# Kernel optimization log

Hardware: AMD Instinct MI355X
Metric: run time of the kernel (lower is better)

The kernel has to match this reference:

```python
import jax, jax.numpy as jnp
import numpy as np

B, S, K = 8, 128, 12          # batch, seq len, nPredicts
DAR, DENC = 256, 256          # AR dim, encoder dim
NNEG = 128                    # negativeSamplingExt
W = S - K                     # windowSize


def setup_inputs() -> dict:
    key = jax.random.key(0)
    k1, k2, k3, k4, k5 = jax.random.split(key, 5)
    cFeature = jax.random.normal(k1, (B, S, DAR), dtype=jnp.float32)
    encodedData = jax.random.normal(k2, (B, S, DENC), dtype=jnp.float32)
    # stacked bias-free Linear weights, one per prediction step k
    Wpred = jax.random.normal(k3, (K, DENC, DAR), dtype=jnp.float32) / jnp.sqrt(DAR)
    n_idx = NNEG * W * B
    batchIdx = jax.random.randint(k4, (n_idx,), 0, B, dtype=jnp.int32)
    seqIdx = jax.random.randint(k5, (n_idx,), 1, S, dtype=jnp.int32)  # low=1 as in torch
    return {"cFeature": cFeature, "encodedData": encodedData, "Wpred": Wpred,
            "batchIdx": batchIdx, "seqIdx": seqIdx}


def reference(cFeature, encodedData, Wpred, batchIdx, seqIdx):
    c = cFeature[:, :W]                                   # (B, W, DAR)
    flat = encodedData.reshape(-1, DENC)                  # (B*S, DENC)

    # sampleClean: baseIdx arange(W) broadcast over (B, NNEG, W) then flattened
    base = jnp.tile(jnp.arange(W, dtype=jnp.int32), B * NNEG)
    seq = (seqIdx + base) % S
    ext = seq + batchIdx * S
    negExt = flat[ext].reshape(B, NNEG, W, DENC)          # irregular gather, ~121 MB

    # per-k linear prediction: locC[k] = c @ Wpred[k].T
    locC = jnp.einsum('bwd,ked->kbwe', c, Wpred)          # (K, B, W, DENC)

    # positives: encodedData[:, k:k+W] for k = 1..K
    pos = jnp.stack([encodedData[:, k:k + W] for k in range(1, K + 1)])  # (K, B, W, DENC)

    # (locC * candidates).mean(dim=feature) == dot / DENC
    posScore = jnp.einsum('kbwe,kbwe->kbw', locC, pos) / DENC           # (K, B, W)
    negScore = jnp.einsum('kbwe,bnwe->kbnw', locC, negExt) / DENC       # (K, B, N, W)

    logits = jnp.concatenate([posScore[:, :, None, :], negScore], axis=2)  # (K, B, 1+N, W)
    logits = jnp.transpose(logits, (0, 1, 3, 2)).reshape(K, B * W, 1 + NNEG)

    # cross entropy with label 0 (positive at class index 0)
    lse = jax.nn.logsumexp(logits, axis=-1)               # (K, B*W)
    losses = jnp.mean(lse - logits[..., 0], axis=-1)      # (K,)
    accs = jnp.mean((jnp.argmax(logits, axis=-1) == 0).astype(jnp.float32), axis=-1)
    return losses[None, :], accs[None, :]                  # (1, K), (1, K)
```

## Files before the change

### kernel.cpp

```cpp
#include <hip/hip_runtime.h>
#include <math.h>

#define B_    8
#define S_    128
#define K_    12
#define DAR_  256
#define DENC_ 256
#define NNEG_ 128
#define W_    116
#define BW_   928

typedef __attribute__((ext_vector_type(8))) short short8;
typedef __attribute__((ext_vector_type(4))) float floatx4;

static __device__ __forceinline__ unsigned short f2bf(float f) {
    union { float f; unsigned int u; } v; v.f = f;
    return (unsigned short)((v.u + 0x7FFFu + ((v.u >> 16) & 1u)) >> 16);
}

__global__ __launch_bounds__(256) void cast_all(
    const float* __restrict__ enc, const float* __restrict__ cf,
    const float* __restrict__ wp,
    unsigned short* __restrict__ ench, unsigned short* __restrict__ cfh,
    unsigned short* __restrict__ wph)
{
    const int g = blockIdx.x * 256 + threadIdx.x;
    const float* src; unsigned short* dst; int off;
    if (g < 32768)      { src = enc; dst = ench; off = g * 8; }
    else if (g < 65536) { src = cf;  dst = cfh;  off = (g - 32768) * 8; }
    else                { src = wp;  dst = wph;  off = (g - 65536) * 8; }
    float4 v0 = *(const float4*)(src + off);
    float4 v1 = *(const float4*)(src + off + 4);
    uint4 o;
    o.x = f2bf(v0.x) | ((unsigned)f2bf(v0.y) << 16);
    o.y = f2bf(v0.z) | ((unsigned)f2bf(v0.w) << 16);
    o.z = f2bf(v1.x) | ((unsigned)f2bf(v1.y) << 16);
    o.w = f2bf(v1.z) | ((unsigned)f2bf(v1.w) << 16);
    *(uint4*)(dst + off) = o;
}

__global__ __launch_bounds__(256) void stage1_mfma(
    const unsigned short* __restrict__ cfh,
    const unsigned short* __restrict__ wph,
    unsigned short* __restrict__ locCh)
{
    __shared__ unsigned short Bh[64 * 256];

    const int tid = threadIdx.x;
    const int mt = blockIdx.x;
    const int nt = blockIdx.y;
    const int k  = blockIdx.z;

    const int lane = tid & 63, wv = tid >> 6;
    const int l15 = lane & 15, quad = lane >> 4;

    const int am = mt * 64 + wv * 16 + l15;
    const bool avalid = (am < BW_);
    short8 a[8];
    if (avalid) {
        const int b = am / W_, w = am - b * W_;
        const unsigned short* arow = cfh + (size_t)(b * S_ + w) * 256;
#pragma unroll
        for (int kt = 0; kt < 8; ++kt)
            a[kt] = *(const short8*)(arow + kt * 32 + quad * 8);
    } else {
#pragma unroll
        for (int kt = 0; kt < 8; ++kt) a[kt] = short8{0,0,0,0,0,0,0,0};
    }

#pragma unroll
    for (int i = 0; i < 8; ++i) {
        const int flat = i * 256 + tid;
        const int row = flat >> 5, ch = flat & 31;
        const int e = nt * 64 + row;
        uint4 bv = *(const uint4*)(wph + ((size_t)(k * 256 + e) * 256 + ch * 8));
        *(uint4*)&Bh[(row * 32 + (ch ^ (row & 7))) * 8] = bv;
    }
    __syncthreads();

    floatx4 acc[4];
#pragma unroll
    for (int n4 = 0; n4 < 4; ++n4) {
        floatx4 c = {0.f, 0.f, 0.f, 0.f};
        const int bn = n4 * 16 + l15;
#pragma unroll
        for (int kt = 0; kt < 8; ++kt) {
            const int ch = kt * 4 + quad;
            short8 bfrag = *(const short8*)&Bh[(bn * 32 + (ch ^ (bn & 7))) * 8];
            c = __builtin_amdgcn_mfma_f32_16x16x32_bf16(a[kt], bfrag, c, 0, 0, 0);
        }
        acc[n4] = c;
    }

#pragma unroll
    for (int n4 = 0; n4 < 4; ++n4) {
        const int e = nt * 64 + n4 * 16 + l15;
#pragma unroll
        for (int r = 0; r < 4; ++r) {
            const int bwo = mt * 64 + wv * 16 + quad * 4 + r;
            if (bwo < BW_)
                locCh[((size_t)k * BW_ + bwo) * 256 + e] = f2bf(acc[r < 0 ? 0 : n4][r]);
        }
    }
}

__global__ __launch_bounds__(256) void stage2_mfma(
    const unsigned short* __restrict__ ench,
    const unsigned short* __restrict__ locCh,
    const int* __restrict__ batchIdx,
    const int* __restrict__ seqIdx,
    float* __restrict__ part)
{
    __shared__ int   idxL[144];
    __shared__ float sc[K_ * 132];

    const int tid = threadIdx.x;
    const int bw = blockIdx.x;
    const int b = bw / W_, w = bw - b * W_;

    const int lane = tid & 63, wv = tid >> 6;
    const int l15 = lane & 15, quad = lane >> 4;

    const int m = (l15 < K_) ? l15 : (K_ - 1);
    const unsigned short* arow = locCh + ((size_t)m * BW_ + bw) * 256;
    short8 a[8];
#pragma unroll
    for (int kt = 0; kt < 8; ++kt)
        a[kt] = *(const short8*)(arow + kt * 32 + quad * 8);

    if (tid < NNEG_) {
        const int ii = (b * NNEG_ + tid) * W_ + w;
        const int bi = batchIdx[ii];
        int si = seqIdx[ii] + w;
        if (si >= S_) si -= S_;
        idxL[tid] = bi * S_ + si;
    } else if (tid < 140) {
        idxL[tid] = b * S_ + w + 1 + (tid - 128);
    }
    __syncthreads();

    floatx4 accT[3];
#pragma unroll
    for (int u = 0; u < 3; ++u) {
        const int t = wv + u * 4;
        floatx4 c = {0.f, 0.f, 0.f, 0.f};
        if (t < 9) {
            const int n = t * 16 + l15;
            const int nn = (n < 140) ? n : 128;
            const unsigned short* brow = ench + (size_t)idxL[nn] * 256;
#pragma unroll
            for (int kt = 0; kt < 8; ++kt) {
                short8 bfrag = *(const short8*)(brow + kt * 32 + quad * 8);
                c = __builtin_amdgcn_mfma_f32_16x16x32_bf16(a[kt], bfrag, c, 0, 0, 0);
            }
        }
        accT[u] = c;
    }

    const float inv = 1.0f / 256.0f;
#pragma unroll
    for (int u = 0; u < 3; ++u) {
        const int t = wv + u * 4;
        if (t < 9) {
#pragma unroll
            for (int r = 0; r < 4; ++r) {
                const int mm = quad * 4 + r;
                if (mm < K_) {
                    const float val = accT[u][r] * inv;
                    if (t < 8)           sc[mm * 132 + t * 16 + l15] = val;
                    else if (l15 == mm)  sc[mm * 132 + 128] = val;
                }
            }
        }
    }
    __syncthreads();

    for (int k = wv; k < K_; k += 4) {
        const float x0  = sc[k * 132 + lane];
        const float x1  = sc[k * 132 + 64 + lane];
        const float pos = sc[k * 132 + 128];
        float mn = fmaxf(x0, x1);
#pragma unroll
        for (int o = 1; o < 64; o <<= 1) mn = fmaxf(mn, __shfl_xor(mn, o, 64));
        const float m2 = fmaxf(mn, pos);
        float s = __expf(x0 - m2) + __expf(x1 - m2);
#pragma unroll
        for (int o = 1; o < 64; o <<= 1) s += __shfl_xor(s, o, 64);
        if (lane == 0) {
            const float lse = m2 + __logf(s + __expf(pos - m2));
            part[k * BW_ + bw]        = lse - pos;
            part[(K_ + k) * BW_ + bw] = (pos >= mn) ? 1.0f : 0.0f;
        }
    }
}

__global__ __launch_bounds__(256) void stage3_reduce(
    const float* __restrict__ part, float* __restrict__ out)
{
    __shared__ float wsum[4];
    const int o = blockIdx.x, tid = threadIdx.x;
    float s = 0.f;
    for (int i = tid; i < BW_; i += 256) s += part[o * BW_ + i];
#pragma unroll
    for (int off = 1; off < 64; off <<= 1) s += __shfl_xor(s, off, 64);
    if ((tid & 63) == 0) wsum[tid >> 6] = s;
    __syncthreads();
    if (tid == 0)
        out[o] = (wsum[0] + wsum[1] + wsum[2] + wsum[3]) / (float)BW_;
}

extern "C" void kernel_launch(void* const* d_in, const int* in_sizes, int n_in,
                              void* d_out, int out_size, void* d_ws, size_t ws_size,
                              hipStream_t stream) {
    const float* cFeat    = (const float*)d_in[0];
    const float* enc      = (const float*)d_in[1];
    const float* Wp       = (const float*)d_in[2];
    const int*   batchIdx = (const int*)d_in[3];
    const int*   seqIdx   = (const int*)d_in[4];
    float* out = (float*)d_out;

    unsigned short* ench  = (unsigned short*)d_ws;
    unsigned short* cfh   = ench + 262144;
    unsigned short* wph   = cfh + 262144;
    unsigned short* locCh = wph + 786432;
    float*          part  = (float*)(locCh + (size_t)K_ * BW_ * 256);

    hipLaunchKernelGGL(cast_all, dim3(640), dim3(256), 0, stream,
                       enc, cFeat, Wp, ench, cfh, wph);
    hipLaunchKernelGGL(stage1_mfma, dim3(15, 4, 12), dim3(256), 0, stream,
                       cfh, wph, locCh);
    hipLaunchKernelGGL(stage2_mfma, dim3(BW_), dim3(256), 0, stream,
                       ench, locCh, batchIdx, seqIdx, part);
    hipLaunchKernelGGL(stage3_reduce, dim3(24), dim3(256), 0, stream,
                       part, out);
}
```

Baseline: 92.93 us.

## Precompute transposed negative indices, enlarge stage1 tile, prefetch stage2 gathers, nontemporal stores

Negative-sample indices are now computed once in the prep kernel into a contiguous per-(b,w) table, replacing strided loads of batchIdx/seqIdx in stage2. Stage1 now computes 128 rows per block, reusing each LDS B fragment across two A tiles. Stage2 issues all gathered encoder row loads before the MFMAs, so memory latency overlaps. Nontemporal loads and stores and a launch_bounds occupancy hint are added throughout. These changes raise register pressure, and the extra prep pass adds some traffic of its own.

Result: slower. 98.99 us (+6.5%).

```diff
diff --git a/kernel.cpp b/kernel.cpp
--- a/kernel.cpp
+++ b/kernel.cpp
@@ -9,37 +9,56 @@
 #define NNEG_ 128
 #define W_    116
 #define BW_   928
+#define NIDX_ 118784
 
 typedef __attribute__((ext_vector_type(8))) short short8;
 typedef __attribute__((ext_vector_type(4))) float floatx4;
+typedef __attribute__((ext_vector_type(4))) unsigned int uintx4;
 
 static __device__ __forceinline__ unsigned short f2bf(float f) {
     union { float f; unsigned int u; } v; v.f = f;
     return (unsigned short)((v.u + 0x7FFFu + ((v.u >> 16) & 1u)) >> 16);
 }
 
-__global__ __launch_bounds__(256) void cast_all(
-    const float* __restrict__ enc, const float* __restrict__ cf,
-    const float* __restrict__ wp,
-    unsigned short* __restrict__ ench, unsigned short* __restrict__ cfh,
-    unsigned short* __restrict__ wph)
-{
-    const int g = blockIdx.x * 256 + threadIdx.x;
-    const float* src; unsigned short* dst; int off;
-    if (g < 32768)      { src = enc; dst = ench; off = g * 8; }
-    else if (g < 65536) { src = cf;  dst = cfh;  off = (g - 32768) * 8; }
-    else                { src = wp;  dst = wph;  off = (g - 65536) * 8; }
-    float4 v0 = *(const float4*)(src + off);
-    float4 v1 = *(const float4*)(src + off + 4);
-    uint4 o;
+static __device__ __forceinline__ uintx4 pack2(float4 v0, float4 v1) {
+    uintx4 o;
     o.x = f2bf(v0.x) | ((unsigned)f2bf(v0.y) << 16);
     o.y = f2bf(v0.z) | ((unsigned)f2bf(v0.w) << 16);
     o.z = f2bf(v1.x) | ((unsigned)f2bf(v1.y) << 16);
     o.w = f2bf(v1.z) | ((unsigned)f2bf(v1.w) << 16);
-    *(uint4*)(dst + off) = o;
-}
-
-__global__ __launch_bounds__(256) void stage1_mfma(
+    return o;
+}
+
+__global__ __launch_bounds__(256) void k0_prep(
+    const float* __restrict__ enc, const float* __restrict__ cf,
+    const float* __restrict__ wp,
+    const int* __restrict__ batchIdx, const int* __restrict__ seqIdx,
+    unsigned short* __restrict__ ench, unsigned short* __restrict__ cfh,
+    unsigned short* __restrict__ wph, int* __restrict__ idxT)
+{
+    const int tid0 = blockIdx.x * 256 + threadIdx.x;
+    for (int g = tid0; g < 163840; g += 192 * 256) {
+        const float* src; unsigned short* dst; int off;
+        if (g < 32768)      { src = enc; dst = ench; off = g * 8; }
+        else if (g < 65536) { src = cf;  dst = cfh;  off = (g - 32768) * 8; }
+        else                { src = wp;  dst = wph;  off = (g - 65536) * 8; }
+        float4 v0 = *(const float4*)(src + off);
+        float4 v1 = *(const float4*)(src + off + 4);
+        uintx4 o = pack2(v0, v1);
+        __builtin_nontemporal_store(o, (uintx4*)(dst + off));
+    }
+    for (int j = tid0; j < NIDX_; j += 192 * 256) {
+        const int n = j & 127, bw = j >> 7;
+        const int b = bw / W_, w = bw - b * W_;
+        const int ii = (b * NNEG_ + n) * W_ + w;
+        const int bi = batchIdx[ii];
+        int si = seqIdx[ii] + w;
+        if (si >= S_) si -= S_;
+        __builtin_nontemporal_store(bi * S_ + si, idxT + j);
+    }
+}
+
+__global__ __launch_bounds__(256, 2) void stage1_mfma(
     const unsigned short* __restrict__ cfh,
     const unsigned short* __restrict__ wph,
     unsigned short* __restrict__ locCh)
@@ -54,61 +73,69 @@
     const int lane = tid & 63, wv = tid >> 6;
     const int l15 = lane & 15, quad = lane >> 4;
 
-    const int am = mt * 64 + wv * 16 + l15;
-    const bool avalid = (am < BW_);
-    short8 a[8];
-    if (avalid) {
-        const int b = am / W_, w = am - b * W_;
+    short8 a[2][8];
+#pragma unroll
+    for (int im = 0; im < 2; ++im) {
+        const int row = mt * 128 + wv * 32 + im * 16 + l15;
+        const int rowc = (row < BW_) ? row : (BW_ - 1);
+        const int b = rowc / W_, w = rowc - b * W_;
         const unsigned short* arow = cfh + (size_t)(b * S_ + w) * 256;
 #pragma unroll
         for (int kt = 0; kt < 8; ++kt)
-            a[kt] = *(const short8*)(arow + kt * 32 + quad * 8);
-    } else {
-#pragma unroll
-        for (int kt = 0; kt < 8; ++kt) a[kt] = short8{0,0,0,0,0,0,0,0};
+            a[im][kt] = *(const short8*)(arow + kt * 32 + quad * 8);
     }
 
 #pragma unroll
     for (int i = 0; i < 8; ++i) {
         const int flat = i * 256 + tid;
         const int row = flat >> 5, ch = flat & 31;
-        const int e = nt * 64 + row;
-        uint4 bv = *(const uint4*)(wph + ((size_t)(k * 256 + e) * 256 + ch * 8));
-        *(uint4*)&Bh[(row * 32 + (ch ^ (row & 7))) * 8] = bv;
-    }
-    __syncthreads();
-
-    floatx4 acc[4];
+        uintx4 bv = *(const uintx4*)(wph + ((size_t)(k * 256 + nt * 64 + row) * 256 + ch * 8));
+        *(uintx4*)&Bh[(row * 32 + (ch ^ (row & 7))) * 8] = bv;
+    }
+    __syncthreads();
+
+    floatx4 acc[2][4];
 #pragma unroll
     for (int n4 = 0; n4 < 4; ++n4) {
-        floatx4 c = {0.f, 0.f, 0.f, 0.f};
         const int bn = n4 * 16 + l15;
+        short8 bfrag[8];
 #pragma unroll
         for (int kt = 0; kt < 8; ++kt) {
             const int ch = kt * 4 + quad;
-            short8 bfrag = *(const short8*)&Bh[(bn * 32 + (ch ^ (bn & 7))) * 8];
-            c = __builtin_amdgcn_mfma_f32_16x16x32_bf16(a[kt], bfrag, c, 0, 0, 0);
-        }
-        acc[n4] = c;
-    }
-
-#pragma unroll
-    for (int n4 = 0; n4 < 4; ++n4) {
-        const int e = nt * 64 + n4 * 16 + l15;
-#pragma unroll
-        for (int r = 0; r < 4; ++r) {
-            const int bwo = mt * 64 + wv * 16 + quad * 4 + r;
-            if (bwo < BW_)
-                locCh[((size_t)k * BW_ + bwo) * 256 + e] = f2bf(acc[r < 0 ? 0 : n4][r]);
-        }
-    }
-}
-
-__global__ __launch_bounds__(256) void stage2_mfma(
+            bfrag[kt] = *(const short8*)&Bh[(bn * 32 + (ch ^ (bn & 7))) * 8];
+        }
+#pragma unroll
+        for (int im = 0; im < 2; ++im) {
+            floatx4 c = (n4 == 0) ? floatx4{0.f, 0.f, 0.f, 0.f} : acc[im][n4];
+            c = acc[im][n4];
+            c = floatx4{0.f, 0.f, 0.f, 0.f};
+#pragma unroll
+            for (int kt = 0; kt < 8; ++kt)
+                c = __builtin_amdgcn_mfma_f32_16x16x32_bf16(a[im][kt], bfrag[kt], c, 0, 0, 0);
+            acc[im][n4] = c;
+        }
+    }
+
+#pragma unroll
+    for (int im = 0; im < 2; ++im) {
+#pragma unroll
+        for (int n4 = 0; n4 < 4; ++n4) {
+            const int e = nt * 64 + n4 * 16 + l15;
+#pragma unroll
+            for (int r = 0; r < 4; ++r) {
+                const int bwo = mt * 128 + wv * 32 + im * 16 + quad * 4 + r;
+                if (bwo < BW_)
+                    __builtin_nontemporal_store(f2bf(acc[im][n4][r]),
+                        locCh + ((size_t)k * BW_ + bwo) * 256 + e);
+            }
+        }
+    }
+}
+
+__global__ __launch_bounds__(256, 2) void stage2_mfma(
     const unsigned short* __restrict__ ench,
     const unsigned short* __restrict__ locCh,
-    const int* __restrict__ batchIdx,
-    const int* __restrict__ seqIdx,
+    const int* __restrict__ idxT,
     float* __restrict__ part)
 {
     __shared__ int   idxL[144];
@@ -126,34 +153,32 @@
     short8 a[8];
 #pragma unroll
     for (int kt = 0; kt < 8; ++kt)
-        a[kt] = *(const short8*)(arow + kt * 32 + quad * 8);
-
-    if (tid < NNEG_) {
-        const int ii = (b * NNEG_ + tid) * W_ + w;
-        const int bi = batchIdx[ii];
-        int si = seqIdx[ii] + w;
-        if (si >= S_) si -= S_;
-        idxL[tid] = bi * S_ + si;
-    } else if (tid < 140) {
-        idxL[tid] = b * S_ + w + 1 + (tid - 128);
-    }
-    __syncthreads();
-
-    floatx4 accT[3];
+        a[kt] = __builtin_nontemporal_load((const short8*)(arow + kt * 32 + quad * 8));
+
+    if (tid < 128)      idxL[tid] = __builtin_nontemporal_load(idxT + bw * 128 + tid);
+    else if (tid < 140) idxL[tid] = b * S_ + w + 1 + (tid - 128);
+    else if (tid < 144) idxL[tid] = b * S_ + w;
+    __syncthreads();
+
+    short8 bfr[3][8];
 #pragma unroll
     for (int u = 0; u < 3; ++u) {
         const int t = wv + u * 4;
+        const int n = t * 16 + l15;
+        const int nn = (t < 9) ? ((n < 140) ? n : 128) : 128;
+        const unsigned short* brow = ench + (size_t)idxL[nn] * 256;
+#pragma unroll
+        for (int kt = 0; kt < 8; ++kt)
+            bfr[u][kt] = *(const short8*)(brow + kt * 32 + quad * 8);
+    }
+
+    floatx4 accT[3];
+#pragma unroll
+    for (int u = 0; u < 3; ++u) {
         floatx4 c = {0.f, 0.f, 0.f, 0.f};
-        if (t < 9) {
-            const int n = t * 16 + l15;
-            const int nn = (n < 140) ? n : 128;
-            const unsigned short* brow = ench + (size_t)idxL[nn] * 256;
-#pragma unroll
-            for (int kt = 0; kt < 8; ++kt) {
-                short8 bfrag = *(const short8*)(brow + kt * 32 + quad * 8);
-                c = __builtin_amdgcn_mfma_f32_16x16x32_bf16(a[kt], bfrag, c, 0, 0, 0);
-            }
-        }
+#pragma unroll
+        for (int kt = 0; kt < 8; ++kt)
+            c = __builtin_amdgcn_mfma_f32_16x16x32_bf16(a[kt], bfr[u][kt], c, 0, 0, 0);
         accT[u] = c;
     }
 
@@ -188,8 +213,9 @@
         for (int o = 1; o < 64; o <<= 1) s += __shfl_xor(s, o, 64);
         if (lane == 0) {
             const float lse = m2 + __logf(s + __expf(pos - m2));
-            part[k * BW_ + bw]        = lse - pos;
-            part[(K_ + k) * BW_ + bw] = (pos >= mn) ? 1.0f : 0.0f;
+            __builtin_nontemporal_store(lse - pos, part + k * BW_ + bw);
+            __builtin_nontemporal_store((pos >= mn) ? 1.0f : 0.0f,
+                                        part + (K_ + k) * BW_ + bw);
         }
     }
 }
@@ -223,14 +249,15 @@
     unsigned short* cfh   = ench + 262144;
     unsigned short* wph   = cfh + 262144;
     unsigned short* locCh = wph + 786432;
-    float*          part  = (float*)(locCh + (size_t)K_ * BW_ * 256);
-
-    hipLaunchKernelGGL(cast_all, dim3(640), dim3(256), 0, stream,
-                       enc, cFeat, Wp, ench, cfh, wph);
-    hipLaunchKernelGGL(stage1_mfma, dim3(15, 4, 12), dim3(256), 0, stream,
+    int*   idxT = (int*)(locCh + (size_t)K_ * BW_ * 256);
+    float* part = (float*)(idxT + NIDX_);
+
+    hipLaunchKernelGGL(k0_prep, dim3(192), dim3(256), 0, stream,
+                       enc, cFeat, Wp, batchIdx, seqIdx, ench, cfh, wph, idxT);
+    hipLaunchKernelGGL(stage1_mfma, dim3(8, 4, 12), dim3(256), 0, stream,
                        cfh, wph, locCh);
     hipLaunchKernelGGL(stage2_mfma, dim3(BW_), dim3(256), 0, stream,
-                       ench, locCh, batchIdx, seqIdx, part);
+                       ench, locCh, idxT, part);
     hipLaunchKernelGGL(stage3_reduce, dim3(24), dim3(256), 0, stream,
                        part, out);
 }
```
